# Kernel tuning notes

Hardware: AMD Instinct MI355X
Metric: run time of the kernel (lower is better)

The kernel has to match this reference:

```python
import jax, jax.numpy as jnp
import numpy as np

B, S, H, A = 64, 2048, 512, 512


def setup_inputs() -> dict:
    key = jax.random.key(0)
    k1, k2, k3, k4, k5 = jax.random.split(key, 5)
    nn_outs = jax.random.normal(k1, (B, S, H), dtype=jnp.float32)
    # lengths in [1, S] so every row has at least one valid step
    batch_lens = jax.random.randint(k2, (B,), 1, S + 1, dtype=jnp.int64)
    # learned params: context vector ~ U(-0.1, 0.1), Linear(H -> A)
    context = jax.random.uniform(k3, (A,), dtype=jnp.float32, minval=-0.1, maxval=0.1)
    proj_w = jax.random.uniform(k4, (A, H), dtype=jnp.float32, minval=-0.1, maxval=0.1)
    proj_b = jax.random.uniform(k5, (A,), dtype=jnp.float32, minval=-0.1, maxval=0.1)
    return {"nn_outs": nn_outs, "batch_lens": batch_lens,
            "context": context, "proj_w": proj_w, "proj_b": proj_b}


def reference(nn_outs, batch_lens, context, proj_w, proj_b):
    # proj = tanh(Linear(nn_outs)): (B, S, A)
    proj = jnp.tanh(jnp.einsum('bsh,ah->bsa', nn_outs, proj_w) + proj_b)
    # attention scores: (B, S)
    scores = jnp.einsum('bsa,a->bs', proj, context)
    # variable-length masked softmax (replaces the per-batch python loop)
    mask = jnp.arange(nn_outs.shape[1])[None, :] < batch_lens[:, None]  # (B, S)
    scores = jnp.where(mask, scores, -jnp.inf)
    atten = jax.nn.softmax(scores, axis=-1)
    atten = jnp.where(mask, atten, 0.0)  # padded positions exactly zero
    # weighted sum over steps: (B, H)
    return jnp.einsum('bs,bsh->bh', atten, nn_outs)
```

## Files before the change

kernel.cpp:

```cpp
#include <hip/hip_runtime.h>

#define BB 64
#define SS 2048
#define HH 512
#define MROWS (BB*SS)

typedef __attribute__((ext_vector_type(8))) short short8;
typedef __attribute__((ext_vector_type(4))) float f32x4;

__device__ inline unsigned short f2bf(float f){
  unsigned int u = __float_as_uint(f);
  u += 0x7FFFu + ((u >> 16) & 1u);
  return (unsigned short)(u >> 16);
}
__device__ inline float bf2f(unsigned short u){
  return __uint_as_float((unsigned int)u << 16);
}

__device__ inline int read_len(const void* lens, int i){
  const int* p = (const int*)lens;
  if (p[1] == 0) return (int)((const long long*)lens)[i];
  return p[i];
}

__device__ inline float fast_tanh(float x){
  x = fminf(fmaxf(x, -15.f), 15.f);
  float e = __expf(2.f * x);
  return (e - 1.f) / (e + 1.f);
}

__device__ inline void gload16(const void* gptr, void* lptr){
  __builtin_amdgcn_global_load_lds(
      (const __attribute__((address_space(1))) void*)gptr,
      (__attribute__((address_space(3))) void*)lptr, 16, 0, 0);
}

__device__ inline short8 cvt8(f32x4 x0, f32x4 x1){
  short8 r;
  r[0] = (short)f2bf(x0[0]); r[1] = (short)f2bf(x0[1]);
  r[2] = (short)f2bf(x0[2]); r[3] = (short)f2bf(x0[3]);
  r[4] = (short)f2bf(x1[0]); r[5] = (short)f2bf(x1[1]);
  r[6] = (short)f2bf(x1[2]); r[7] = (short)f2bf(x1[3]);
  return r;
}

__global__ __launch_bounds__(256) void convw_kernel(
    const float* __restrict__ W, unsigned short* __restrict__ Wb)
{
  size_t base = (size_t)blockIdx.x * 64 * HH;
  int t = threadIdx.x;
  #pragma unroll
  for (int j = 0; j < 32; j++) {
    size_t idx = base + (size_t)j * 1024 + t * 4;
    float4 v = *(const float4*)(W + idx);
    unsigned int p0 = (unsigned int)f2bf(v.x) | ((unsigned int)f2bf(v.y) << 16);
    unsigned int p1 = (unsigned int)f2bf(v.z) | ((unsigned int)f2bf(v.w) << 16);
    *(uint2*)(Wb + idx) = make_uint2(p0, p1);
  }
}

__global__ __launch_bounds__(256) void scores_mfma(
    const float* __restrict__ X, const unsigned short* __restrict__ Wb,
    const void* __restrict__ lens, const float* __restrict__ ctx,
    const float* __restrict__ pb, float* __restrict__ sp)
{
  int bid = blockIdx.x;
  int wg = (bid & 7) * 512 + (bid >> 3);
  int ntile = wg & 3;
  int mtile = wg >> 2;
  int s_start = (mtile * 128) & (SS - 1);
  int b = (mtile * 128) >> 11;
  if (s_start >= read_len(lens, b)) return;

  __shared__ __align__(16) float          Asf[128 * 64];
  __shared__ __align__(16) unsigned short Bs[128 * 64];

  int tid = threadIdx.x;
  int lane = tid & 63;
  int w = tid >> 6;
  int wm = w >> 1, wn = w & 1;
  int l15 = lane & 15, g = lane >> 4;

  f32x4 acc[4][4];
  #pragma unroll
  for (int i = 0; i < 4; i++)
    #pragma unroll
    for (int j = 0; j < 4; j++) acc[i][j] = (f32x4)0.f;

  int arow_off = lane >> 4;
  int ap = lane & 15;
  int brow = lane >> 3;
  int bgrp = (lane & 7) ^ brow;
  const unsigned short* Brow = Wb + ((size_t)(ntile * 128) + w * 8 + brow) * HH + bgrp * 8;

  const float* Abase = X + (size_t)(mtile * 128) * HH;

  for (int kt = 0; kt < HH; kt += 64) {
    #pragma unroll
    for (int i = 0; i < 8; i++) {
      int row = w * 32 + i * 4 + arow_off;
      int g16 = ap ^ (row & 15);
      gload16(Abase + (size_t)row * HH + kt + g16 * 4,
              &Asf[(w * 32 + i * 4) * 64]);
    }
    #pragma unroll
    for (int i = 0; i < 4; i++) {
      gload16(Brow + (size_t)(i * 32) * HH + kt, &Bs[(i * 32 + w * 8) * 64]);
    }
    __syncthreads();
    #pragma unroll
    for (int kk = 0; kk < 64; kk += 32) {
      short8 af[4], bfr[4];
      int ga0 = (kk >> 2) + 2 * g;
      #pragma unroll
      for (int im = 0; im < 4; im++) {
        int r = wm * 64 + im * 16 + l15;
        f32x4 x0 = *(const f32x4*)&Asf[r * 64 + ((ga0)     ^ l15) * 4];
        f32x4 x1 = *(const f32x4*)&Asf[r * 64 + ((ga0 + 1) ^ l15) * 4];
        af[im] = cvt8(x0, x1);
      }
      int gb = g + (kk >> 3);
      #pragma unroll
      for (int in = 0; in < 4; in++) {
        int r = wn * 64 + in * 16 + l15;
        int pg = gb ^ (r & 7);
        bfr[in] = *(const short8*)&Bs[r * 64 + pg * 8];
      }
      #pragma unroll
      for (int im = 0; im < 4; im++)
        #pragma unroll
        for (int in = 0; in < 4; in++)
          acc[im][in] = __builtin_amdgcn_mfma_f32_16x16x32_bf16(
              af[im], bfr[in], acc[im][in], 0, 0, 0);
    }
    __syncthreads();
  }

  float pbv[4], ctxv[4];
  #pragma unroll
  for (int in = 0; in < 4; in++) {
    int a_g = ntile * 128 + wn * 64 + in * 16 + l15;
    pbv[in] = pb[a_g];
    ctxv[in] = ctx[a_g];
  }
  #pragma unroll
  for (int im = 0; im < 4; im++) {
    #pragma unroll
    for (int r = 0; r < 4; r++) {
      float rowsum = 0.f;
      #pragma unroll
      for (int in = 0; in < 4; in++)
        rowsum += fast_tanh(acc[im][in][r] + pbv[in]) * ctxv[in];
      #pragma unroll
      for (int m = 1; m < 16; m <<= 1)
        rowsum += __shfl_xor(rowsum, m, 64);
      if (l15 == 0) {
        int rowg = mtile * 128 + wm * 64 + im * 16 + g * 4 + r;
        sp[(size_t)(ntile * 2 + wn) * MROWS + rowg] = rowsum;
      }
    }
  }
}

__global__ __launch_bounds__(256) void softmax_kernel(
    const float* __restrict__ sp, const void* __restrict__ lens,
    float* __restrict__ wts)
{
  int b = blockIdx.x;
  int tid = threadIdx.x;
  int len = read_len(lens, b);
  float sc[8];
  #pragma unroll
  for (int i = 0; i < 8; i++) {
    int s = tid + i * 256;
    size_t row = (size_t)b * SS + s;
    float v = 0.f;
    #pragma unroll
    for (int p = 0; p < 8; p++) v += sp[(size_t)p * MROWS + row];
    sc[i] = v;
  }
  float m = -1e30f;
  #pragma unroll
  for (int i = 0; i < 8; i++)
    if (tid + i * 256 < len) m = fmaxf(m, sc[i]);
  #pragma unroll
  for (int off = 1; off < 64; off <<= 1) m = fmaxf(m, __shfl_xor(m, off, 64));
  __shared__ float redm[4];
  __shared__ float reds[4];
  int w = tid >> 6, lane = tid & 63;
  if (lane == 0) redm[w] = m;
  __syncthreads();
  m = fmaxf(fmaxf(redm[0], redm[1]), fmaxf(redm[2], redm[3]));
  float e[8]; float sum = 0.f;
  #pragma unroll
  for (int i = 0; i < 8; i++) {
    int s = tid + i * 256;
    e[i] = (s < len) ? __expf(sc[i] - m) : 0.f;
    sum += e[i];
  }
  #pragma unroll
  for (int off = 1; off < 64; off <<= 1) sum += __shfl_xor(sum, off, 64);
  if (lane == 0) reds[w] = sum;
  __syncthreads();
  sum = reds[0] + reds[1] + reds[2] + reds[3];
  float inv = 1.f / sum;
  #pragma unroll
  for (int i = 0; i < 8; i++) {
    int s = tid + i * 256;
    wts[(size_t)b * SS + s] = e[i] * inv;
  }
}

__global__ __launch_bounds__(256) void wsum_kernel(
    const float* __restrict__ X, const float* __restrict__ wts,
    const void* __restrict__ lens, float* __restrict__ op)
{
  int sc = blockIdx.x;
  int b  = blockIdx.y;
  int tid = threadIdx.x;
  int s0 = sc * 128;
  int len = read_len(lens, b);
  int cnt = min(128, len - s0);
  float* o = op + ((size_t)sc * BB + b) * HH;
  if (cnt <= 0) {
    *(float2*)(o + tid * 2) = make_float2(0.f, 0.f);
    return;
  }
  __shared__ float wsh[128];
  __shared__ f32x4 red[128];
  if (tid < 128) wsh[tid] = wts[(size_t)b * SS + s0 + tid];
  __syncthreads();
  int h = (tid & 127) * 4;
  int sr = tid >> 7;
  f32x4 acc = (f32x4)0.f;
  for (int i = sr; i < cnt; i += 2) {
    float wv = wsh[i];
    const float* xr = X + ((size_t)b * SS + s0 + i) * HH + h;
    float4 xv = *(const float4*)xr;
    acc[0] += wv * xv.x;
    acc[1] += wv * xv.y;
    acc[2] += wv * xv.z;
    acc[3] += wv * xv.w;
  }
  if (sr == 1) red[tid & 127] = acc;
  __syncthreads();
  if (sr == 0) {
    f32x4 r2 = red[tid];
    acc[0] += r2[0]; acc[1] += r2[1]; acc[2] += r2[2]; acc[3] += r2[3];
    *(f32x4*)(o + h) = acc;
  }
}

__global__ __launch_bounds__(512) void reduce_kernel(
    const float* __restrict__ op, float* __restrict__ out)
{
  int b = blockIdx.x;
  int h = threadIdx.x;
  float v = 0.f;
  #pragma unroll
  for (int sc = 0; sc < 16; sc++) v += op[((size_t)sc * BB + b) * HH + h];
  out[(size_t)b * HH + h] = v;
}

__global__ __launch_bounds__(256) void scores_fb(
    const float* __restrict__ X, const void* __restrict__ lens,
    const float* __restrict__ ctx, const float* __restrict__ W,
    const float* __restrict__ pb, float* __restrict__ sp)
{
  int bid = blockIdx.x;
  int wg = (bid & 7) * 512 + (bid >> 3);
  int ntile = wg & 3;
  int mtile = wg >> 2;
  int s_start = (mtile * 128) & (SS - 1);
  int b = (mtile * 128) >> 11;
  if (s_start >= read_len(lens, b)) return;

  __shared__ unsigned short As[128 * 72];
  __shared__ unsigned short Bs[128 * 72];

  int tid = threadIdx.x;
  int lane = tid & 63;
  int w = tid >> 6;
  int wm = w >> 1, wn = w & 1;
  int l15 = lane & 15, g = lane >> 4;

  f32x4 acc[4][4];
  #pragma unroll
  for (int i = 0; i < 4; i++)
    #pragma unroll
    for (int j = 0; j < 4; j++) acc[i][j] = (f32x4)0.f;

  int srow = tid >> 4;
  int scol = (tid & 15) * 4;
  const float* Xbase = X + (size_t)(mtile * 128) * HH;
  const float* Wbase = W + (size_t)(ntile * 128) * HH;

  for (int kt = 0; kt < HH; kt += 64) {
    #pragma unroll
    for (int i = 0; i < 8; i++) {
      int row = srow + i * 16;
      float4 va = *(const float4*)(Xbase + (size_t)row * HH + kt + scol);
      unsigned int p0 = (unsigned int)f2bf(va.x) | ((unsigned int)f2bf(va.y) << 16);
      unsigned int p1 = (unsigned int)f2bf(va.z) | ((unsigned int)f2bf(va.w) << 16);
      *(uint2*)&As[row * 72 + scol] = make_uint2(p0, p1);
      float4 vb = *(const float4*)(Wbase + (size_t)row * HH + kt + scol);
      unsigned int q0 = (unsigned int)f2bf(vb.x) | ((unsigned int)f2bf(vb.y) << 16);
      unsigned int q1 = (unsigned int)f2bf(vb.z) | ((unsigned int)f2bf(vb.w) << 16);
      *(uint2*)&Bs[row * 72 + scol] = make_uint2(q0, q1);
    }
    __syncthreads();
    #pragma unroll
    for (int kk = 0; kk < 64; kk += 32) {
      short8 af[4], bfr[4];
      int ko = kk + g * 8;
      #pragma unroll
      for (int im = 0; im < 4; im++)
        af[im] = *(const short8*)&As[(wm * 64 + im * 16 + l15) * 72 + ko];
      #pragma unroll
      for (int in = 0; in < 4; in++)
        bfr[in] = *(const short8*)&Bs[(wn * 64 + in * 16 + l15) * 72 + ko];
      #pragma unroll
      for (int im = 0; im < 4; im++)
        #pragma unroll
        for (int in = 0; in < 4; in++)
          acc[im][in] = __builtin_amdgcn_mfma_f32_16x16x32_bf16(
              af[im], bfr[in], acc[im][in], 0, 0, 0);
    }
    __syncthreads();
  }

  #pragma unroll
  for (int im = 0; im < 4; im++) {
    #pragma unroll
    for (int r = 0; r < 4; r++) {
      float rowsum = 0.f;
      #pragma unroll
      for (int in = 0; in < 4; in++) {
        int a_g = ntile * 128 + wn * 64 + in * 16 + l15;
        rowsum += fast_tanh(acc[im][in][r] + pb[a_g]) * ctx[a_g];
      }
      #pragma unroll
      for (int m = 1; m < 16; m <<= 1)
        rowsum += __shfl_xor(rowsum, m, 64);
      if (l15 == 0) {
        int rowg = mtile * 128 + wm * 64 + im * 16 + g * 4 + r;
        sp[(size_t)(ntile * 2 + wn) * MROWS + rowg] = rowsum;
      }
    }
  }
}

extern "C" void kernel_launch(void* const* d_in, const int* in_sizes, int n_in,
                              void* d_out, int out_size, void* d_ws, size_t ws_size,
                              hipStream_t stream) {
  const float* X   = (const float*)d_in[0];
  const void*  lens = d_in[1];
  const float* ctx = (const float*)d_in[2];
  const float* W   = (const float*)d_in[3];
  const float* pb  = (const float*)d_in[4];
  float* out = (float*)d_out;

  char* ws = (char*)d_ws;
  const size_t WB_BYTES = (size_t)HH * HH * 2;
  const size_t SP_BYTES = 8ull * MROWS * 4;
  const size_t WT_BYTES = (size_t)BB * SS * 4;
  const size_t OP_BYTES = 16ull * BB * HH * 4;
  const size_t NEED = WB_BYTES + SP_BYTES + WT_BYTES + OP_BYTES;

  if (ws_size >= NEED) {
    unsigned short* Wb = (unsigned short*)ws;
    float* sp  = (float*)(ws + WB_BYTES);
    float* wts = (float*)(ws + WB_BYTES + SP_BYTES);
    float* op  = (float*)(ws + WB_BYTES + SP_BYTES + WT_BYTES);

    convw_kernel<<<8, 256, 0, stream>>>(W, Wb);
    scores_mfma<<<4096, 256, 0, stream>>>(X, Wb, lens, ctx, pb, sp);
    softmax_kernel<<<BB, 256, 0, stream>>>(sp, lens, wts);
    wsum_kernel<<<dim3(16, BB), 256, 0, stream>>>(X, wts, lens, op);
    reduce_kernel<<<BB, 512, 0, stream>>>(op, out);
  } else {
    float* sp  = (float*)ws;
    float* wts = (float*)(ws + SP_BYTES);
    float* op  = (float*)(ws + SP_BYTES + WT_BYTES);

    scores_fb<<<4096, 256, 0, stream>>>(X, lens, ctx, W, pb, sp);
    softmax_kernel<<<BB, 256, 0, stream>>>(sp, lens, wts);
    wsum_kernel<<<dim3(16, BB), 256, 0, stream>>>(X, wts, lens, op);
    reduce_kernel<<<BB, 512, 0, stream>>>(op, out);
  }
}
```

Measured before the change: 143.4 us.

## Double-buffer LDS tiles and convert A to bf16 once before staging

The scores GEMM now loads the fp32 A tile into registers, converts it to bf16 once per element, and writes bf16 into a double-buffered LDS tile. The B tile is also double-buffered with async global-to-LDS loads, so the next K-tile's loads overlap the current MFMA work and each iteration needs one barrier instead of two. This removes the redundant fp32-to-bf16 conversion that each wave repeated on shared A data, and halves the A footprint in LDS. It adds register pressure from holding the prefetched fp32 A tile, partly offset by the launch bound requesting two blocks per CU.

```diff
diff --git a/kernel.cpp b/kernel.cpp
--- a/kernel.cpp
+++ b/kernel.cpp
@@ -13,9 +13,6 @@
   u += 0x7FFFu + ((u >> 16) & 1u);
   return (unsigned short)(u >> 16);
 }
-__device__ inline float bf2f(unsigned short u){
-  return __uint_as_float((unsigned int)u << 16);
-}
 
 __device__ inline int read_len(const void* lens, int i){
   const int* p = (const int*)lens;
@@ -35,12 +32,12 @@
       (__attribute__((address_space(3))) void*)lptr, 16, 0, 0);
 }
 
-__device__ inline short8 cvt8(f32x4 x0, f32x4 x1){
+__device__ inline short8 cvt8p(float4 x0, float4 x1){
   short8 r;
-  r[0] = (short)f2bf(x0[0]); r[1] = (short)f2bf(x0[1]);
-  r[2] = (short)f2bf(x0[2]); r[3] = (short)f2bf(x0[3]);
-  r[4] = (short)f2bf(x1[0]); r[5] = (short)f2bf(x1[1]);
-  r[6] = (short)f2bf(x1[2]); r[7] = (short)f2bf(x1[3]);
+  r[0] = (short)f2bf(x0.x); r[1] = (short)f2bf(x0.y);
+  r[2] = (short)f2bf(x0.z); r[3] = (short)f2bf(x0.w);
+  r[4] = (short)f2bf(x1.x); r[5] = (short)f2bf(x1.y);
+  r[6] = (short)f2bf(x1.z); r[7] = (short)f2bf(x1.w);
   return r;
 }
 
@@ -59,7 +56,7 @@
   }
 }
 
-__global__ __launch_bounds__(256) void scores_mfma(
+__global__ __launch_bounds__(256, 2) void scores_mfma(
     const float* __restrict__ X, const unsigned short* __restrict__ Wb,
     const void* __restrict__ lens, const float* __restrict__ ctx,
     const float* __restrict__ pb, float* __restrict__ sp)
@@ -72,8 +69,8 @@
   int b = (mtile * 128) >> 11;
   if (s_start >= read_len(lens, b)) return;
 
-  __shared__ __align__(16) float          Asf[128 * 64];
-  __shared__ __align__(16) unsigned short Bs[128 * 64];
+  __shared__ __align__(16) unsigned short As[2][128 * 64];
+  __shared__ __align__(16) unsigned short Bs[2][128 * 64];
 
   int tid = threadIdx.x;
   int lane = tid & 63;
@@ -87,44 +84,55 @@
     #pragma unroll
     for (int j = 0; j < 4; j++) acc[i][j] = (f32x4)0.f;
 
-  int arow_off = lane >> 4;
-  int ap = lane & 15;
+  int arow = tid >> 1;
+  int alg0 = (tid & 1) * 4;
+  const float* Ag = X + (size_t)(mtile * 128 + arow) * HH;
+  int apg[4];
+  #pragma unroll
+  for (int j = 0; j < 4; j++) apg[j] = (alg0 + j) ^ (arow & 7);
+
   int brow = lane >> 3;
   int bgrp = (lane & 7) ^ brow;
-  const unsigned short* Brow = Wb + ((size_t)(ntile * 128) + w * 8 + brow) * HH + bgrp * 8;
-
-  const float* Abase = X + (size_t)(mtile * 128) * HH;
-
-  for (int kt = 0; kt < HH; kt += 64) {
-    #pragma unroll
-    for (int i = 0; i < 8; i++) {
-      int row = w * 32 + i * 4 + arow_off;
-      int g16 = ap ^ (row & 15);
-      gload16(Abase + (size_t)row * HH + kt + g16 * 4,
-              &Asf[(w * 32 + i * 4) * 64]);
-    }
-    #pragma unroll
-    for (int i = 0; i < 4; i++) {
-      gload16(Brow + (size_t)(i * 32) * HH + kt, &Bs[(i * 32 + w * 8) * 64]);
-    }
-    __syncthreads();
+  const unsigned short* Bg = Wb + ((size_t)(ntile * 128) + w * 8 + brow) * HH + bgrp * 8;
+
+  float4 ar[8];
+
+#define A_ISSUE(KT) { _Pragma("unroll") for (int j = 0; j < 4; j++) { \
+    const float* p = Ag + (KT) + (alg0 + j) * 8; \
+    ar[2*j]   = *(const float4*)p; \
+    ar[2*j+1] = *(const float4*)(p + 4); } }
+
+#define A_WRITE(BUF) { _Pragma("unroll") for (int j = 0; j < 4; j++) { \
+    *(short8*)&As[BUF][arow * 64 + apg[j] * 8] = cvt8p(ar[2*j], ar[2*j+1]); } }
+
+#define B_ISSUE(BUF, KT) { _Pragma("unroll") for (int i = 0; i < 4; i++) { \
+    gload16(Bg + (size_t)(i * 32) * HH + (KT), &Bs[BUF][(i * 32 + w * 8) * 64]); } }
+
+  A_ISSUE(0)
+  B_ISSUE(0, 0)
+  A_WRITE(0)
+  __syncthreads();
+
+  for (int t = 0; t < 8; ++t) {
+    int cur = t & 1;
+    int nxt = cur ^ 1;
+    if (t < 7) {
+      A_ISSUE((t + 1) * 64)
+      B_ISSUE(nxt, (t + 1) * 64)
+    }
     #pragma unroll
     for (int kk = 0; kk < 64; kk += 32) {
       short8 af[4], bfr[4];
-      int ga0 = (kk >> 2) + 2 * g;
+      int ga = g + (kk >> 3);
       #pragma unroll
       for (int im = 0; im < 4; im++) {
         int r = wm * 64 + im * 16 + l15;
-        f32x4 x0 = *(const f32x4*)&Asf[r * 64 + ((ga0)     ^ l15) * 4];
-        f32x4 x1 = *(const f32x4*)&Asf[r * 64 + ((ga0 + 1) ^ l15) * 4];
-        af[im] = cvt8(x0, x1);
+        af[im] = *(const short8*)&As[cur][r * 64 + ((ga ^ (r & 7))) * 8];
       }
-      int gb = g + (kk >> 3);
       #pragma unroll
       for (int in = 0; in < 4; in++) {
         int r = wn * 64 + in * 16 + l15;
-        int pg = gb ^ (r & 7);
-        bfr[in] = *(const short8*)&Bs[r * 64 + pg * 8];
+        bfr[in] = *(const short8*)&Bs[cur][r * 64 + ((ga ^ (r & 7))) * 8];
       }
       #pragma unroll
       for (int im = 0; im < 4; im++)
@@ -133,6 +141,7 @@
           acc[im][in] = __builtin_amdgcn_mfma_f32_16x16x32_bf16(
               af[im], bfr[in], acc[im][in], 0, 0, 0);
     }
+    if (t < 7) A_WRITE(nxt)
     __syncthreads();
   }
 
```

Result: slower. 178.6 us (+24.6%).
